# Kernel optimization log

Measured on AMD Instinct MI355X. Metric: run time of the kernel, lower is better.

The kernel has to match this reference:

```python
import jax, jax.numpy as jnp
import numpy as np

N_HEADS = 16
D_EMBED = 1024
BATCH = 1
SEQ = 4096


def setup_inputs() -> dict:
    key = jax.random.key(0)
    ks = jax.random.split(key, 5)
    d = D_EMBED
    x = jax.random.normal(ks[0], (BATCH, SEQ, d), dtype=jnp.float32)
    # torch Linear weights stored as (in, out) so y = x @ W + b
    W_in = jax.random.normal(ks[1], (d, 3 * d), dtype=jnp.float32) / np.sqrt(d)
    b_in = jax.random.normal(ks[2], (3 * d,), dtype=jnp.float32) * 0.02
    W_out = jax.random.normal(ks[3], (d, d), dtype=jnp.float32) / np.sqrt(d)
    b_out = jax.random.normal(ks[4], (d,), dtype=jnp.float32) * 0.02
    return {"x": x, "W_in": W_in, "b_in": b_in, "W_out": W_out, "b_out": b_out}


def reference(x, W_in, b_in, W_out, b_out):
    B, S, d = x.shape
    H = N_HEADS
    dh = d // H
    qkv = x @ W_in + b_in                      # [B, S, 3d]
    q, k, v = jnp.split(qkv, 3, axis=-1)       # each [B, S, d]
    # [B, S, H, dh] -> [B, H, S, dh]
    q = q.reshape(B, S, H, dh).transpose(0, 2, 1, 3)
    k = k.reshape(B, S, H, dh).transpose(0, 2, 1, 3)
    v = v.reshape(B, S, H, dh).transpose(0, 2, 1, 3)
    scores = jnp.einsum("bhqd,bhkd->bhqk", q, k) / jnp.sqrt(jnp.float32(dh))
    causal = jnp.tril(jnp.ones((S, S), dtype=bool))  # True = keep
    scores = jnp.where(causal, scores, -jnp.inf)
    attn = jax.nn.softmax(scores, axis=-1)
    out = jnp.einsum("bhqk,bhkd->bhqd", attn, v)     # [B, H, S, dh]
    out = out.transpose(0, 2, 1, 3).reshape(B, S, d)
    return out @ W_out + b_out
```

## Files before the change

### kernel.cpp

```cpp
#include <hip/hip_runtime.h>
#include <stdint.h>

#define S_LEN 4096
#define D_EMB 1024
#define NH 16
#define DHEAD 64
#define N3 3072

typedef __attribute__((ext_vector_type(8))) short short8;
typedef __attribute__((ext_vector_type(4))) short short4v;
typedef __attribute__((ext_vector_type(4))) float f32x4;

#define OFF_XB    0u
#define OFF_WINT  4194304u
#define OFF_WOUTT 7340032u
#define OFF_Q     8388608u
#define OFF_ATTN  20971520u

#define QSCALE 0.1803368801111204f
#define DEFER_THR 11.0f

__device__ __forceinline__ unsigned short f2bf(float f) {
  unsigned u = __float_as_uint(f);
  unsigned r = u + 0x7FFFu + ((u >> 16) & 1u);
  return (unsigned short)(r >> 16);
}
__device__ __forceinline__ unsigned cvtpk_bf16(float lo, float hi) {
  unsigned r;
  asm("v_cvt_pk_bf16_f32 %0, %1, %2" : "=v"(r) : "v"(lo), "v"(hi));
  return r;
}
__device__ __forceinline__ void gload16(const void* g, void* l) {
  __builtin_amdgcn_global_load_lds((const __attribute__((address_space(1))) void*)g,
                                   (__attribute__((address_space(3))) void*)l, 16, 0, 0);
}

__global__ __launch_bounds__(256) void prep_kernel(const float* __restrict__ x,
                                                   const float* __restrict__ W_in,
                                                   const float* __restrict__ W_out,
                                                   ushort* __restrict__ xb,
                                                   ushort* __restrict__ wint,
                                                   ushort* __restrict__ woutt) {
  __shared__ float tile[32][33];
  int b = blockIdx.x;
  if (b < 4096) {
    int i = (b * 256 + threadIdx.x) * 4;
    float4 v = *(const float4*)(x + i);
    ushort4 o;
    o.x = f2bf(v.x); o.y = f2bf(v.y); o.z = f2bf(v.z); o.w = f2bf(v.w);
    *(ushort4*)(xb + i) = o;
    return;
  }
  const float* src;
  ushort* dst;
  int R, C, bx, by;
  if (b < 7168) {
    int t = b - 4096;
    src = W_in; dst = wint; R = D_EMB; C = N3;
    bx = t % 96; by = t / 96;
  } else {
    int t = b - 7168;
    src = W_out; dst = woutt; R = D_EMB; C = D_EMB;
    bx = t & 31; by = t >> 5;
  }
  int tx = threadIdx.x & 31, ty = threadIdx.x >> 5;
  int c0 = bx * 32, r0 = by * 32;
#pragma unroll
  for (int i = 0; i < 32; i += 8)
    tile[ty + i][tx] = src[(size_t)(r0 + ty + i) * C + c0 + tx];
  __syncthreads();
#pragma unroll
  for (int i = 0; i < 32; i += 8)
    dst[(size_t)(c0 + ty + i) * R + r0 + tx] = f2bf(tile[tx][ty + i]);
}

__global__ __launch_bounds__(512, 2) void gemm1_8phase(const ushort* __restrict__ A,
                                                       const ushort* __restrict__ Bt,
                                                       const float* __restrict__ bias,
                                                       ushort* __restrict__ o16) {
  __shared__ ushort L[65536];
  const int K = 1024;
  int tid = threadIdx.x, w = tid >> 6, lane = tid & 63;
  int wr = w >> 2, wc = w & 3;
  int l15 = lane & 15, g = lane >> 4;
  int lr = lane >> 3, lc = lane & 7;
  int swcol = (lc ^ lr) * 8;
  int rxor = (l15 & 7) << 3;
  int id = blockIdx.y * 12 + blockIdx.x;
  int id2 = (id & 7) * 24 + (id >> 3);
  int bm = (id2 / 12) * 256, bn = (id2 % 12) * 256;

  f32x4 acc[8][4];
#pragma unroll
  for (int m = 0; m < 8; ++m)
#pragma unroll
    for (int n = 0; n < 4; ++n) acc[m][n] = (f32x4){0.f, 0.f, 0.f, 0.f};

  auto stageA = [&](int t, int h) {
#pragma unroll
    for (int r2 = 0; r2 < 2; ++r2)
      gload16(A + (size_t)(bm + h * 128 + r2 * 64 + w * 8 + lr) * K + t * 64 + swcol,
              &L[((t & 1) * 2 + h) * 8192 + r2 * 4096 + w * 512]);
  };
  auto stageB = [&](int t, int h) {
#pragma unroll
    for (int r2 = 0; r2 < 2; ++r2)
      gload16(Bt + (size_t)(bn + h * 128 + r2 * 64 + w * 8 + lr) * K + t * 64 + swcol,
              &L[32768 + ((t & 1) * 2 + h) * 8192 + r2 * 4096 + w * 512]);
  };

  short8 bf[4][2], af[2][2];
  auto readB = [&](int tb) {
    int base = 32768 + (tb * 2 + (wc >> 1)) * 8192 + (wc & 1) * 4096;
#pragma unroll
    for (int n = 0; n < 4; ++n)
#pragma unroll
      for (int ks = 0; ks < 2; ++ks)
        bf[n][ks] = *(const short8*)&L[base + (n * 16 + l15) * 64 + ((ks * 32 + g * 8) ^ rxor)];
  };
  auto readA2 = [&](int tb, int m0) {
    int base = (tb * 2 + wr) * 8192;
#pragma unroll
    for (int mi = 0; mi < 2; ++mi)
#pragma unroll
      for (int ks = 0; ks < 2; ++ks)
        af[mi][ks] = *(const short8*)&L[base + ((m0 + mi) * 16 + l15) * 64 + ((ks * 32 + g * 8) ^ rxor)];
  };
  auto mfma8 = [&](int m0) {
#pragma unroll
    for (int mi = 0; mi < 2; ++mi)
#pragma unroll
      for (int n = 0; n < 4; ++n)
#pragma unroll
        for (int ks = 0; ks < 2; ++ks)
          acc[m0 + mi][n] =
              __builtin_amdgcn_mfma_f32_16x16x32_bf16(af[mi][ks], bf[n][ks], acc[m0 + mi][n], 0, 0, 0);
  };

#define BAR() __builtin_amdgcn_s_barrier()
#define LGK0() asm volatile("s_waitcnt lgkmcnt(0)" ::: "memory")
#define VM4() asm volatile("s_waitcnt vmcnt(4)" ::: "memory")
#define VM0() asm volatile("s_waitcnt vmcnt(0)" ::: "memory")

  stageA(0, 0); stageA(0, 1); stageB(0, 0); stageB(0, 1);
  stageB(1, 0); stageB(1, 1);
  VM4();
  BAR();

  for (int i = 0; i < 8; ++i) {
    int T = 2 * i;
    bool more = (T + 2 < 16);
    readB(0); readA2(0, 0); stageA(T + 1, 0);
    BAR(); LGK0();
    __builtin_amdgcn_s_setprio(1); mfma8(0); __builtin_amdgcn_s_setprio(0);
    BAR();
    readA2(0, 2); stageA(T + 1, 1);
    BAR(); LGK0();
    __builtin_amdgcn_s_setprio(1); mfma8(2); __builtin_amdgcn_s_setprio(0);
    BAR();
    readA2(0, 4); if (more) stageB(T + 2, 0);
    BAR(); LGK0();
    __builtin_amdgcn_s_setprio(1); mfma8(4); __builtin_amdgcn_s_setprio(0);
    BAR();
    readA2(0, 6); if (more) stageB(T + 2, 1);
    BAR(); LGK0();
    __builtin_amdgcn_s_setprio(1); mfma8(6); __builtin_amdgcn_s_setprio(0);
    if (more) VM4(); else VM0();
    BAR();
    readB(1); readA2(1, 0); if (more) stageA(T + 2, 0);
    BAR(); LGK0();
    __builtin_amdgcn_s_setprio(1); mfma8(0); __builtin_amdgcn_s_setprio(0);
    BAR();
    readA2(1, 2); if (more) stageA(T + 2, 1);
    BAR(); LGK0();
    __builtin_amdgcn_s_setprio(1); mfma8(2); __builtin_amdgcn_s_setprio(0);
    BAR();
    readA2(1, 4); if (more) stageB(T + 3, 0);
    BAR(); LGK0();
    __builtin_amdgcn_s_setprio(1); mfma8(4); __builtin_amdgcn_s_setprio(0);
    BAR();
    readA2(1, 6); if (more) stageB(T + 3, 1);
    BAR(); LGK0();
    __builtin_amdgcn_s_setprio(1); mfma8(6); __builtin_amdgcn_s_setprio(0);
    if (more) VM4(); else VM0();
    BAR();
  }
#undef BAR
#undef LGK0
#undef VM4
#undef VM0

#pragma unroll
  for (int m = 0; m < 8; ++m) {
    int rbase = bm + wr * 128 + m * 16 + g * 4;
#pragma unroll
    for (int n = 0; n < 4; ++n) {
      int c = bn + wc * 64 + n * 16 + l15;
      float bv = bias[c];
      int which = c >> 10, cc = c & 1023, hh = cc >> 6, dcol = cc & 63;
      if (which == 2) {
        ushort4 o;
        o.x = f2bf(acc[m][n][0] + bv);
        o.y = f2bf(acc[m][n][1] + bv);
        o.z = f2bf(acc[m][n][2] + bv);
        o.w = f2bf(acc[m][n][3] + bv);
        *(ushort4*)&o16[8388608u + (size_t)hh * (DHEAD * (size_t)S_LEN) +
                        (size_t)dcol * S_LEN + rbase] = o;
      } else {
        float qs = (which == 0) ? QSCALE : 1.0f;
        ushort* dst = o16 + (size_t)which * 4194304u +
                      (size_t)hh * (S_LEN * DHEAD) + dcol;
#pragma unroll
        for (int j = 0; j < 4; ++j)
          dst[(size_t)(rbase + j) * DHEAD] = f2bf((acc[m][n][j] + bv) * qs);
      }
    }
  }
}

#define BK 64

__global__ __launch_bounds__(256) void gemm2_kernel(const ushort* __restrict__ A,
                                                    const ushort* __restrict__ Bt,
                                                    const float* __restrict__ bias,
                                                    float* __restrict__ o32,
                                                    int N, int K) {
  __shared__ ushort As[128 * 64];
  __shared__ ushort Bs[64 * 64];
  int tid = threadIdx.x, w = tid >> 6, lane = tid & 63;
  int wr = w >> 1, wc = w & 1;
  int l15 = lane & 15, g = lane >> 4;
  int gx = gridDim.x;
  int id = blockIdx.y * gx + blockIdx.x;
  int q8 = (gx * gridDim.y) >> 3;
  int id2 = (id & 7) * q8 + (id >> 3);
  int bm = (id2 / gx) * 128, bn = (id2 % gx) * 64;
  f32x4 acc[4][2];
#pragma unroll
  for (int m = 0; m < 4; ++m)
#pragma unroll
    for (int n = 0; n < 2; ++n) acc[m][n] = (f32x4){0.f, 0.f, 0.f, 0.f};

  int srow = lane >> 3;
  int scol = (lane & 7) * 8;

  for (int k0 = 0; k0 < K; k0 += BK) {
    __syncthreads();
#pragma unroll
    for (int i = 0; i < 4; ++i) {
      int ch = w * 4 + i;
      gload16(A + (size_t)(bm + ch * 8 + srow) * K + k0 + scol, &As[ch * 512]);
    }
#pragma unroll
    for (int i = 0; i < 2; ++i) {
      int ch = w * 2 + i;
      gload16(Bt + (size_t)(bn + ch * 8 + srow) * K + k0 + scol, &Bs[ch * 512]);
    }
    __syncthreads();
    short8 a[4][2], b[2][2];
#pragma unroll
    for (int m = 0; m < 4; ++m)
#pragma unroll
      for (int t = 0; t < 2; ++t)
        a[m][t] = *(const short8*)&As[(wr * 64 + m * 16 + l15) * 64 + t * 32 + g * 8];
#pragma unroll
    for (int n = 0; n < 2; ++n)
#pragma unroll
      for (int t = 0; t < 2; ++t)
        b[n][t] = *(const short8*)&Bs[(wc * 32 + n * 16 + l15) * 64 + t * 32 + g * 8];
#pragma unroll
    for (int m = 0; m < 4; ++m)
#pragma unroll
      for (int n = 0; n < 2; ++n)
#pragma unroll
        for (int t = 0; t < 2; ++t)
          acc[m][n] = __builtin_amdgcn_mfma_f32_16x16x32_bf16(a[m][t], b[n][t], acc[m][n], 0, 0, 0);
  }

#pragma unroll
  for (int m = 0; m < 4; ++m) {
    int rbase = bm + wr * 64 + m * 16 + g * 4;
#pragma unroll
    for (int n = 0; n < 2; ++n) {
      int c = bn + wc * 32 + n * 16 + l15;
      float bv = bias[c];
#pragma unroll
      for (int j = 0; j < 4; ++j)
        o32[(size_t)(rbase + j) * N + c] = acc[m][n][j] + bv;
    }
  }
}

__global__ __launch_bounds__(512) void attn_kernel(const ushort* __restrict__ Q,
                                                   const ushort* __restrict__ Kg,
                                                   const ushort* __restrict__ Vtg,
                                                   ushort* __restrict__ O) {
  __shared__ ushort Ks[2][64 * 64];
  __shared__ ushort Vs[2][64 * 64];
  int bid = blockIdx.x;
  int h = bid & 15;
  int qt = (bid < 256) ? (31 - (bid >> 4)) : ((bid - 256) >> 4);
  int q0 = qt * 128;
  int tid = threadIdx.x, w = tid >> 6, lane = tid & 63;
  int l15 = lane & 15, g = lane >> 4;
  const ushort* qh = Q + (size_t)h * (S_LEN * DHEAD);
  const ushort* kh = Kg + (size_t)h * (S_LEN * DHEAD);
  const ushort* vh = Vtg + (size_t)h * (DHEAD * (size_t)S_LEN);
  int srow = w * 8 + (lane >> 3);
  int sgcol = (((lane & 7) ^ ((lane >> 3) & 7))) * 8;
  ushort* kdst0 = &Ks[0][w * 512];  ushort* kdst1 = &Ks[1][w * 512];
  ushort* vdst0 = &Vs[0][w * 512];  ushort* vdst1 = &Vs[1][w * 512];
  int kxor = (l15 & 7) << 4;
  int koff0 = ((g * 16) ^ kxor) >> 1;
  int koff1 = ((64 + g * 16) ^ kxor) >> 1;
  int voff[4];
#pragma unroll
  for (int ct = 0; ct < 4; ++ct) voff[ct] = ((ct * 32 + g * 8) ^ kxor) >> 1;

  int qrow = q0 + w * 16 + l15;
  short8 aq[2];
#pragma unroll
  for (int t = 0; t < 2; ++t)
    aq[t] = *(const short8*)&qh[(size_t)qrow * DHEAD + t * 32 + g * 8];

  f32x4 acc_o[4];
#pragma unroll
  for (int dt = 0; dt < 4; ++dt) acc_o[dt] = (f32x4){0.f, 0.f, 0.f, 0.f};
  float m = -1e30f, l = 0.f;
  int last = 2 * qt + 1;

  gload16(&kh[(size_t)srow * DHEAD + sgcol], kdst0);
  gload16(&vh[(size_t)srow * S_LEN + sgcol], vdst0);
  asm volatile("s_waitcnt vmcnt(0)" ::: "memory");
  __syncthreads();
  int cur = 0;

  for (int it = 0; it <= last; ++it) {
    int kv0 = it * 64;
    bool more = (it < last);
    const ushort* Kc = Ks[cur];
    const ushort* Vc = Vs[cur];

    if (more) {
      int kv1 = kv0 + 64;
      gload16(&kh[(size_t)(kv1 + srow) * DHEAD + sgcol], cur ? kdst0 : kdst1);
      gload16(&vh[(size_t)srow * S_LEN + kv1 + sgcol], cur ? vdst0 : vdst1);
    }

    f32x4 accs[4];
#pragma unroll
    for (int ct = 0; ct < 4; ++ct) accs[ct] = (f32x4){0.f, 0.f, 0.f, 0.f};
    __builtin_amdgcn_s_setprio(1);
#pragma unroll
    for (int ct = 0; ct < 4; ++ct) {
      int rb = (ct * 16 + l15) * 64;
      short8 kf0 = *(const short8*)&Kc[rb + koff0];
      short8 kf1 = *(const short8*)&Kc[rb + koff1];
      accs[ct] = __builtin_amdgcn_mfma_f32_16x16x32_bf16(kf0, aq[0], accs[ct], 0, 0, 0);
      accs[ct] = __builtin_amdgcn_mfma_f32_16x16x32_bf16(kf1, aq[1], accs[ct], 0, 0, 0);
    }
    __builtin_amdgcn_s_setprio(0);

    if (it >= 2 * qt) {
#pragma unroll
      for (int ct = 0; ct < 4; ++ct) {
        int kbase = kv0 + ct * 16 + g * 4;
#pragma unroll
        for (int j = 0; j < 4; ++j)
          if (kbase + j > qrow) accs[ct][j] = -1e30f;
      }
    }

    float a0 = fmaxf(fmaxf(accs[0][0], accs[0][1]), fmaxf(accs[0][2], accs[0][3]));
    float a1 = fmaxf(fmaxf(accs[1][0], accs[1][1]), fmaxf(accs[1][2], accs[1][3]));
    float a2 = fmaxf(fmaxf(accs[2][0], accs[2][1]), fmaxf(accs[2][2], accs[2][3]));
    float a3 = fmaxf(fmaxf(accs[3][0], accs[3][1]), fmaxf(accs[3][2], accs[3][3]));
    float pm = fmaxf(fmaxf(a0, a1), fmaxf(a2, a3));

    if (!__all(pm <= m + DEFER_THR)) {
      pm = fmaxf(pm, __shfl_xor(pm, 16));
      pm = fmaxf(pm, __shfl_xor(pm, 32));
      float mnew = fmaxf(m, pm);
      float corr = __builtin_amdgcn_exp2f(m - mnew);
      l *= corr; m = mnew;
#pragma unroll
      for (int dt = 0; dt < 4; ++dt)
#pragma unroll
        for (int j = 0; j < 4; ++j) acc_o[dt][j] *= corr;
    }

    float rs = 0.f;
    short8 pk8[2];
#pragma unroll
    for (int t2 = 0; t2 < 2; ++t2) {
      float p0 = __builtin_amdgcn_exp2f(accs[2 * t2][0] - m);
      float p1 = __builtin_amdgcn_exp2f(accs[2 * t2][1] - m);
      float p2 = __builtin_amdgcn_exp2f(accs[2 * t2][2] - m);
      float p3 = __builtin_amdgcn_exp2f(accs[2 * t2][3] - m);
      float p4 = __builtin_amdgcn_exp2f(accs[2 * t2 + 1][0] - m);
      float p5 = __builtin_amdgcn_exp2f(accs[2 * t2 + 1][1] - m);
      float p6 = __builtin_amdgcn_exp2f(accs[2 * t2 + 1][2] - m);
      float p7 = __builtin_amdgcn_exp2f(accs[2 * t2 + 1][3] - m);
      rs += ((p0 + p1) + (p2 + p3)) + ((p4 + p5) + (p6 + p7));
      union { unsigned u[4]; short8 v; } pu;
      pu.u[0] = cvtpk_bf16(p0, p1);
      pu.u[1] = cvtpk_bf16(p2, p3);
      pu.u[2] = cvtpk_bf16(p4, p5);
      pu.u[3] = cvtpk_bf16(p6, p7);
      pk8[t2] = pu.v;
    }
    l += rs;

    __builtin_amdgcn_s_setprio(1);
#pragma unroll
    for (int dt = 0; dt < 4; ++dt) {
      int rb = (dt * 16 + l15) * 64;
#pragma unroll
      for (int t2 = 0; t2 < 2; ++t2) {
        union { short4v hh[2]; short8 v; } vu;
        vu.hh[0] = *(const short4v*)&Vc[rb + voff[2 * t2]];
        vu.hh[1] = *(const short4v*)&Vc[rb + voff[2 * t2 + 1]];
        acc_o[dt] = __builtin_amdgcn_mfma_f32_16x16x32_bf16(vu.v, pk8[t2], acc_o[dt], 0, 0, 0);
      }
    }
    __builtin_amdgcn_s_setprio(0);

    asm volatile("s_waitcnt vmcnt(0)" ::: "memory");
    __syncthreads();
    cur ^= 1;
  }

  l += __shfl_xor(l, 16);
  l += __shfl_xor(l, 32);
  float rl = (l > 0.f) ? 1.f / l : 0.f;
#pragma unroll
  for (int dt = 0; dt < 4; ++dt) {
    ushort4 o;
    o.x = f2bf(acc_o[dt][0] * rl);
    o.y = f2bf(acc_o[dt][1] * rl);
    o.z = f2bf(acc_o[dt][2] * rl);
    o.w = f2bf(acc_o[dt][3] * rl);
    *(ushort4*)&O[(size_t)qrow * D_EMB + h * DHEAD + dt * 16 + g * 4] = o;
  }
}

extern "C" void kernel_launch(void* const* d_in, const int* in_sizes, int n_in,
                              void* d_out, int out_size, void* d_ws, size_t ws_size,
                              hipStream_t stream) {
  const float* x = (const float*)d_in[0];
  const float* W_in = (const float*)d_in[1];
  const float* b_in = (const float*)d_in[2];
  const float* W_out = (const float*)d_in[3];
  const float* b_out = (const float*)d_in[4];
  float* out = (float*)d_out;
  ushort* ws = (ushort*)d_ws;

  prep_kernel<<<8192, 256, 0, stream>>>(x, W_in, W_out,
                                        ws + OFF_XB, ws + OFF_WINT, ws + OFF_WOUTT);
  gemm1_8phase<<<dim3(12, 16), 512, 0, stream>>>(
      ws + OFF_XB, ws + OFF_WINT, b_in, ws + OFF_Q);
  attn_kernel<<<512, 512, 0, stream>>>(
      ws + OFF_Q, ws + OFF_Q + 4194304u, ws + OFF_Q + 8388608u, ws + OFF_ATTN);
  gemm2_kernel<<<dim3(16, 32), 256, 0, stream>>>(
      ws + OFF_ATTN, ws + OFF_WOUTT, b_out, out, D_EMB, D_EMB);
}
```

Baseline: 134.7 us.

## Triple-buffer output projection GEMM with swizzled LDS and async prefetch

Rewrites gemm2_kernel's main loop to use a three-stage LDS ring buffer. Global-to-LDS loads run two tiles ahead, and manual vmcnt waits with a single barrier per iteration replace the two __syncthreads. LDS columns are XOR-swizzled to cut bank conflicts on the fragment reads, and the MFMA block runs at raised wave priority. It hardcodes K=1024 (NT=16) and raises LDS use, which may reduce occupancy.

Result: faster. 125.0 us (-7.3%).

```diff
diff --git a/kernel.cpp b/kernel.cpp
--- a/kernel.cpp
+++ b/kernel.cpp
@@ -218,18 +218,18 @@
   }
 }
 
-#define BK 64
-
 __global__ __launch_bounds__(256) void gemm2_kernel(const ushort* __restrict__ A,
                                                     const ushort* __restrict__ Bt,
                                                     const float* __restrict__ bias,
                                                     float* __restrict__ o32,
                                                     int N, int K) {
-  __shared__ ushort As[128 * 64];
-  __shared__ ushort Bs[64 * 64];
+  __shared__ ushort L[36864];
   int tid = threadIdx.x, w = tid >> 6, lane = tid & 63;
   int wr = w >> 1, wc = w & 1;
   int l15 = lane & 15, g = lane >> 4;
+  int lr = lane >> 3, lc = lane & 7;
+  int swcol = (lc ^ lr) * 8;
+  int rxor = (l15 & 7) << 3;
   int gx = gridDim.x;
   int id = blockIdx.y * gx + blockIdx.x;
   int q8 = (gx * gridDim.y) >> 3;
@@ -241,40 +241,58 @@
 #pragma unroll
     for (int n = 0; n < 2; ++n) acc[m][n] = (f32x4){0.f, 0.f, 0.f, 0.f};
 
-  int srow = lane >> 3;
-  int scol = (lane & 7) * 8;
-
-  for (int k0 = 0; k0 < K; k0 += BK) {
-    __syncthreads();
+  auto stage = [&](int t) {
+    int buf = t % 3;
 #pragma unroll
     for (int i = 0; i < 4; ++i) {
       int ch = w * 4 + i;
-      gload16(A + (size_t)(bm + ch * 8 + srow) * K + k0 + scol, &As[ch * 512]);
+      gload16(A + (size_t)(bm + ch * 8 + lr) * K + t * 64 + swcol,
+              &L[buf * 8192 + ch * 512]);
     }
 #pragma unroll
     for (int i = 0; i < 2; ++i) {
       int ch = w * 2 + i;
-      gload16(Bt + (size_t)(bn + ch * 8 + srow) * K + k0 + scol, &Bs[ch * 512]);
-    }
-    __syncthreads();
+      gload16(Bt + (size_t)(bn + ch * 8 + lr) * K + t * 64 + swcol,
+              &L[24576 + buf * 4096 + ch * 512]);
+    }
+  };
+
+  const int NT = 16;
+  stage(0); stage(1);
+  asm volatile("s_waitcnt vmcnt(6)" ::: "memory");
+  __builtin_amdgcn_s_barrier();
+
+  for (int t = 0; t < NT; ++t) {
+    int buf = t % 3;
+    if (t + 2 < NT) stage(t + 2);
+    const ushort* Ab = &L[buf * 8192];
+    const ushort* Bb = &L[24576 + buf * 4096];
     short8 a[4][2], b[2][2];
 #pragma unroll
     for (int m = 0; m < 4; ++m)
 #pragma unroll
-      for (int t = 0; t < 2; ++t)
-        a[m][t] = *(const short8*)&As[(wr * 64 + m * 16 + l15) * 64 + t * 32 + g * 8];
+      for (int ks = 0; ks < 2; ++ks)
+        a[m][ks] = *(const short8*)&Ab[(wr * 64 + m * 16 + l15) * 64 + ((ks * 32 + g * 8) ^ rxor)];
 #pragma unroll
     for (int n = 0; n < 2; ++n)
 #pragma unroll
-      for (int t = 0; t < 2; ++t)
-        b[n][t] = *(const short8*)&Bs[(wc * 32 + n * 16 + l15) * 64 + t * 32 + g * 8];
+      for (int ks = 0; ks < 2; ++ks)
+        b[n][ks] = *(const short8*)&Bb[(wc * 32 + n * 16 + l15) * 64 + ((ks * 32 + g * 8) ^ rxor)];
+    asm volatile("s_waitcnt lgkmcnt(0)" ::: "memory");
+    __builtin_amdgcn_s_setprio(1);
 #pragma unroll
     for (int m = 0; m < 4; ++m)
 #pragma unroll
       for (int n = 0; n < 2; ++n)
 #pragma unroll
-        for (int t = 0; t < 2; ++t)
-          acc[m][n] = __builtin_amdgcn_mfma_f32_16x16x32_bf16(a[m][t], b[n][t], acc[m][n], 0, 0, 0);
+        for (int ks = 0; ks < 2; ++ks)
+          acc[m][n] = __builtin_amdgcn_mfma_f32_16x16x32_bf16(a[m][ks], b[n][ks], acc[m][n], 0, 0, 0);
+    __builtin_amdgcn_s_setprio(0);
+    if (t + 2 < NT)
+      asm volatile("s_waitcnt vmcnt(6)" ::: "memory");
+    else if (t + 1 < NT)
+      asm volatile("s_waitcnt vmcnt(0)" ::: "memory");
+    __builtin_amdgcn_s_barrier();
   }
 
 #pragma unroll
```
